# Performance work log

Measured on AMD Instinct MI355X. Metric: run time of the kernel, lower is better.

## Reference

```python
import jax, jax.numpy as jnp
import numpy as np

GRID_SIZE = 8
SPLINE_ORDER = 3  # cubic B-splines
GRID_MIN, GRID_MAX = -1.0, 1.0


def _make_grid():
    # Extended knot vector: grid_size + 2*order intervals -> G+2k+1 knots
    h = (GRID_MAX - GRID_MIN) / GRID_SIZE
    n = GRID_SIZE + 2 * SPLINE_ORDER + 1
    return jnp.asarray(GRID_MIN - SPLINE_ORDER * h + h * np.arange(n, dtype=np.float32))


def bspline_basis(x, grid, k):
    # x: (B, in) -> (B, in, G+k) via Cox-de Boor recursion
    x = x[..., None]
    b = ((x >= grid[:-1]) & (x < grid[1:])).astype(x.dtype)
    for p in range(1, k + 1):
        left = (x - grid[: -(p + 1)]) / (grid[p:-1] - grid[: -(p + 1)]) * b[..., :-1]
        right = (grid[p + 1:] - x) / (grid[p + 1:] - grid[1:-p]) * b[..., 1:]
        b = left + right
    return b


def setup_inputs() -> dict:
    key = jax.random.key(0)
    k1, k2, k3 = jax.random.split(key, 3)
    B, IN, OUT = 32768, 256, 256
    NB = GRID_SIZE + SPLINE_ORDER  # 11
    x = jax.random.normal(k1, (B, IN), dtype=jnp.float32)
    ln_gamma = jnp.ones((IN,), dtype=jnp.float32)
    ln_beta = jnp.zeros((IN,), dtype=jnp.float32)
    coeff = jax.random.normal(k2, (OUT, IN, NB), dtype=jnp.float32) * 0.1
    base_w = jax.random.normal(k3, (OUT, IN), dtype=jnp.float32) * (1.0 / np.sqrt(IN))
    return {"x": x, "ln_gamma": ln_gamma, "ln_beta": ln_beta, "coeff": coeff, "base_w": base_w}


def reference(x, ln_gamma, ln_beta, coeff, base_w):
    grid = _make_grid()
    # LayerNorm over in_features (eps = torch default 1e-5)
    mu = jnp.mean(x, axis=-1, keepdims=True)
    var = jnp.mean(jnp.square(x - mu), axis=-1, keepdims=True)
    normalized = (x - mu) * jax.lax.rsqrt(var + 1e-5) * ln_gamma + ln_beta
    # Spline branch: basis expansion (B, in, nb) contracted with coeff (out, in, nb)
    basis = bspline_basis(normalized, grid, SPLINE_ORDER)
    spline = jnp.einsum('bin,oin->bo', basis, coeff)
    # Base branch: SiLU(x) @ W^T (note: uses raw x, not normalized)
    base = jnp.einsum('bi,oi->bo', jax.nn.silu(x), base_w)
    return spline + base
```

## Files before the change

kernel.cpp:

```cpp
#include <hip/hip_runtime.h>
#include <hip/hip_bf16.h>

typedef _Float16 f16x8 __attribute__((ext_vector_type(8)));
typedef float f32x4 __attribute__((ext_vector_type(4)));

#define BM 128
#define BKH 96
#define NCHUNK 32
#define IN_F 256
#define OUT_F 256
#define KDIM 3072

__device__ inline void async_b16(const void* g, void* l) {
  __builtin_amdgcn_global_load_lds(
      (const __attribute__((address_space(1))) unsigned int*)g,
      (__attribute__((address_space(3))) unsigned int*)l, 16, 0, 0);
}

static __device__ inline unsigned pack2(float a, float b) {
  union { _Float16 h[2]; unsigned u; } t;
  t.h[0] = (_Float16)a;
  t.h[1] = (_Float16)b;
  return t.u;
}

__global__ __launch_bounds__(256) void prep_w(const float* __restrict__ coeff,
                                              const float* __restrict__ base_w,
                                              _Float16* __restrict__ W2F) {
  const int u   = blockIdx.x * 256 + threadIdx.x;
  const int c   = u / 3072;
  const int r   = u % 3072;
  const int bcb = r / 192;
  const int r2  = r % 192;
  const int g   = r2 / 64;
  const int ln  = r2 % 64;
  const int o   = bcb * 16 + (ln & 15);
  const int k8  = g * 4 + (ln >> 4);
  const int kh0 = c * 96 + k8 * 8;
  _Float16 h[8];
  #pragma unroll
  for (int e = 0; e < 8; ++e) {
    const int k = kh0 + e;
    const int i = k / 12, m = k % 12;
    const float v = (m == 11) ? base_w[o * IN_F + i] : coeff[(o * IN_F + i) * 11 + m];
    h[e] = (_Float16)v;
  }
  *(f16x8*)&W2F[(size_t)u * 8] = *(const f16x8*)h;
}

__global__ __launch_bounds__(512, 2) void kan_fused(const float* __restrict__ x,
                                                    const float* __restrict__ gamma,
                                                    const float* __restrict__ beta,
                                                    const _Float16* __restrict__ W2F,
                                                    float* __restrict__ out) {
  __shared__ _Float16 A0[24 * 512], A1[24 * 512];
  __shared__ _Float16 B0[48 * 512], B1[48 * 512];
  __shared__ float mu_s[BM], rs_s[BM];

  const int tid  = threadIdx.x;
  const int lane = tid & 63;
  const int wid  = tid >> 6;
  const int row0 = blockIdx.x * BM;

  for (int rr = wid; rr < BM; rr += 8) {
    const float4 v = *(const float4*)(x + (size_t)(row0 + rr) * IN_F + lane * 4);
    float s  = v.x + v.y + v.z + v.w;
    float sq = v.x * v.x + v.y * v.y + v.z * v.z + v.w * v.w;
    #pragma unroll
    for (int off = 32; off >= 1; off >>= 1) {
      s  += __shfl_xor(s, off);
      sq += __shfl_xor(sq, off);
    }
    if (lane == 0) {
      const float mu  = s * (1.0f / 256.0f);
      const float var = sq * (1.0f / 256.0f) - mu * mu;
      mu_s[rr] = mu;
      rs_s[rr] = 1.0f / sqrtf(var + 1e-5f);
    }
  }
  __syncthreads();

  const int wr   = wid >> 2;
  const int wc   = wid & 3;
  const int lrow = lane & 15;

  f32x4 acc[4][4] = {};

  const int plrow = tid & 15;
  const int pfq   = (tid >> 4) & 3;
  const int prb   = tid >> 6;
  const int prow  = prb * 16 + plrow;
  const float mu = mu_s[prow], rs = rs_s[prow];
  const float* xrow = x + (size_t)(row0 + prow) * IN_F + pfq * 2;
  const float* grow = gamma + pfq * 2;
  const float* brow = beta + pfq * 2;

  int aoff0, aoff1, aoff2;
  {
    const int k80 = pfq * 3 + 0, k81 = pfq * 3 + 1, k82 = pfq * 3 + 2;
    aoff0 = (prb * 3 + (k80 >> 2)) * 512 + (k80 & 3) * 128 + plrow * 8;
    aoff1 = (prb * 3 + (k81 >> 2)) * 512 + (k81 & 3) * 128 + plrow * 8;
    aoff2 = (prb * 3 + (k82 >> 2)) * 512 + (k82 & 3) * 128 + plrow * 8;
  }

  const char* const wsrc = (const char*)W2F + (size_t)wid * 6144 + (size_t)lane * 16;
  auto stageB = [&](int c, _Float16* Bb) {
    const char* gb = wsrc + (size_t)c * 49152;
    char* lb = (char*)Bb + wid * 6144;
    #pragma unroll
    for (int j = 0; j < 6; ++j)
      async_b16(gb + j * 1024, lb + j * 1024);
  };

  auto produce = [&](_Float16* buf, float2 xv, float2 gv, float2 bv) {
    unsigned R[12];
    #pragma unroll
    for (int q = 0; q < 2; ++q) {
      const float xr = q ? xv.y : xv.x;
      const float gq = q ? gv.y : gv.x;
      const float bq = q ? bv.y : bv.x;
      const float n  = (xr - mu) * rs * gq + bq;
      const float v  = (n + 1.75f) * 4.0f;
      const float fj = floorf(v);
      const float u  = v - fj;
      const float u2 = u * u, u3 = u2 * u;
      const float w0 = (1.0f / 6.0f) * (1.0f - 3.0f * u + 3.0f * u2 - u3);
      const float w1 = (1.0f / 6.0f) * (3.0f * u3 - 6.0f * u2 + 4.0f);
      const float w2 = (1.0f / 6.0f) * (-3.0f * u3 + 3.0f * u2 + 3.0f * u + 1.0f);
      const float w3 = (1.0f / 6.0f) * u3;
      const unsigned W0 = pack2(w0, w1);
      const unsigned W1 = pack2(w2, w3);
      const int p    = (int)fj - 3;
      const bool odd = (p & 1);
      const unsigned v0 = odd ? (W0 << 16) : W0;
      const unsigned v1 = odd ? ((W0 >> 16) | (W1 << 16)) : W1;
      const unsigned v2 = odd ? (W1 >> 16) : 0u;
      const int s0 = (v >= 0.0f && v < 14.0f) ? (p >> 1) : 99;
      const int s1 = s0 + 1, s2 = s0 + 2;
      #pragma unroll
      for (int k = 0; k < 6; ++k) {
        unsigned r = (k == s0) ? v0 : 0u;
        r = (k == s1) ? v1 : r;
        r = (k == s2) ? v2 : r;
        R[q * 6 + k] = r;
      }
      const float sl = xr * __builtin_amdgcn_rcpf(1.0f + __expf(-xr));
      R[q * 6 + 5] = (R[q * 6 + 5] & 0x0000FFFFu) | pack2(0.0f, sl);
    }
    *(f16x8*)&buf[aoff0] = *(const f16x8*)&R[0];
    *(f16x8*)&buf[aoff1] = *(const f16x8*)&R[4];
    *(f16x8*)&buf[aoff2] = *(const f16x8*)&R[8];
  };

  auto domfma = [&](const _Float16* Ab, const _Float16* Bb) {
    #pragma unroll
    for (int fk = 0; fk < 3; ++fk) {
      f16x8 a[4], b[4];
      #pragma unroll
      for (int fm = 0; fm < 4; ++fm)
        a[fm] = *(const f16x8*)&Ab[((wr * 4 + fm) * 3 + fk) * 512 + lane * 8];
      #pragma unroll
      for (int fn = 0; fn < 4; ++fn)
        b[fn] = *(const f16x8*)&Bb[((wc * 4 + fn) * 3 + fk) * 512 + lane * 8];
      #pragma unroll
      for (int fm = 0; fm < 4; ++fm)
        #pragma unroll
        for (int fn = 0; fn < 4; ++fn)
          acc[fm][fn] = __builtin_amdgcn_mfma_f32_16x16x32_f16(a[fm], b[fn], acc[fm][fn], 0, 0, 0);
    }
  };

  stageB(0, B0);
  float2 xv0 = *(const float2*)(xrow);
  float2 gv0 = *(const float2*)(grow);
  float2 bv0 = *(const float2*)(brow);
  float2 xv1 = *(const float2*)(xrow + 8);
  float2 gv1 = *(const float2*)(grow + 8);
  float2 bv1 = *(const float2*)(brow + 8);
  produce(A0, xv0, gv0, bv0);
  __syncthreads();

  for (int c = 0; c < NCHUNK; c += 2) {
    const int cp2 = (c + 2 < NCHUNK) ? (c + 2) : (NCHUNK - 1);
    const int cp3 = (c + 3 < NCHUNK) ? (c + 3) : (NCHUNK - 1);
    stageB(c + 1, B1);
    xv0 = *(const float2*)(xrow + cp2 * 8);
    gv0 = *(const float2*)(grow + cp2 * 8);
    bv0 = *(const float2*)(brow + cp2 * 8);
    if (wid & 1) { domfma(A0, B0); produce(A1, xv1, gv1, bv1); }
    else         { produce(A1, xv1, gv1, bv1); domfma(A0, B0); }
    __syncthreads();
    stageB(cp2, B0);
    xv1 = *(const float2*)(xrow + cp3 * 8);
    gv1 = *(const float2*)(grow + cp3 * 8);
    bv1 = *(const float2*)(brow + cp3 * 8);
    if (wid & 1) { domfma(A1, B1); produce(A0, xv0, gv0, bv0); }
    else         { produce(A0, xv0, gv0, bv0); domfma(A1, B1); }
    __syncthreads();
  }

  const int orow0 = row0 + wr * 64 + (lane >> 4) * 4;
  const int ocol0 = wc * 64 + lrow;
  #pragma unroll
  for (int fm = 0; fm < 4; ++fm)
    #pragma unroll
    for (int fn = 0; fn < 4; ++fn)
      #pragma unroll
      for (int r = 0; r < 4; ++r)
        out[(size_t)(orow0 + fm * 16 + r) * OUT_F + ocol0 + fn * 16] = acc[fm][fn][r];
}

extern "C" void kernel_launch(void* const* d_in, const int* in_sizes, int n_in,
                              void* d_out, int out_size, void* d_ws, size_t ws_size,
                              hipStream_t stream) {
  const float* x      = (const float*)d_in[0];
  const float* gamma  = (const float*)d_in[1];
  const float* beta   = (const float*)d_in[2];
  const float* coeff  = (const float*)d_in[3];
  const float* base_w = (const float*)d_in[4];
  float* out = (float*)d_out;
  _Float16* W2F = (_Float16*)d_ws;

  prep_w<<<dim3(384), dim3(256), 0, stream>>>(coeff, base_w, W2F);
  kan_fused<<<dim3(32768 / BM), dim3(512), 0, stream>>>(x, gamma, beta, W2F, out);
}
```

Baseline: 81.42 us.

## Load weight fragments directly from global into registers, bypassing LDS

Removes the LDS staging of the weight (B) tiles via global_load_lds. Each wave now loads its own B fragments straight from global memory into register double buffers (bA/bB), and the MFMA loop reads B from registers. This cuts LDS traffic and frees LDS, and the launch bound no longer requests 2 blocks per CU. In exchange, waves that share a column group load the same weights redundantly from global/L2, and register pressure rises by 24 f16x8 vectors, which may limit occupancy.

New measurement: 92.75 us. 1.14x slower.

```diff
diff --git a/kernel.cpp b/kernel.cpp
--- a/kernel.cpp
+++ b/kernel.cpp
@@ -5,17 +5,10 @@
 typedef float f32x4 __attribute__((ext_vector_type(4)));
 
 #define BM 128
-#define BKH 96
 #define NCHUNK 32
 #define IN_F 256
 #define OUT_F 256
 #define KDIM 3072
-
-__device__ inline void async_b16(const void* g, void* l) {
-  __builtin_amdgcn_global_load_lds(
-      (const __attribute__((address_space(1))) unsigned int*)g,
-      (__attribute__((address_space(3))) unsigned int*)l, 16, 0, 0);
-}
 
 static __device__ inline unsigned pack2(float a, float b) {
   union { _Float16 h[2]; unsigned u; } t;
@@ -48,13 +41,12 @@
   *(f16x8*)&W2F[(size_t)u * 8] = *(const f16x8*)h;
 }
 
-__global__ __launch_bounds__(512, 2) void kan_fused(const float* __restrict__ x,
-                                                    const float* __restrict__ gamma,
-                                                    const float* __restrict__ beta,
-                                                    const _Float16* __restrict__ W2F,
-                                                    float* __restrict__ out) {
+__global__ __launch_bounds__(512) void kan_fused(const float* __restrict__ x,
+                                                 const float* __restrict__ gamma,
+                                                 const float* __restrict__ beta,
+                                                 const _Float16* __restrict__ W2F,
+                                                 float* __restrict__ out) {
   __shared__ _Float16 A0[24 * 512], A1[24 * 512];
-  __shared__ _Float16 B0[48 * 512], B1[48 * 512];
   __shared__ float mu_s[BM], rs_s[BM];
 
   const int tid  = threadIdx.x;
@@ -103,13 +95,14 @@
     aoff2 = (prb * 3 + (k82 >> 2)) * 512 + (k82 & 3) * 128 + plrow * 8;
   }
 
-  const char* const wsrc = (const char*)W2F + (size_t)wid * 6144 + (size_t)lane * 16;
-  auto stageB = [&](int c, _Float16* Bb) {
-    const char* gb = wsrc + (size_t)c * 49152;
-    char* lb = (char*)Bb + wid * 6144;
-    #pragma unroll
-    for (int j = 0; j < 6; ++j)
-      async_b16(gb + j * 1024, lb + j * 1024);
+  const char* const wbsrc = (const char*)W2F + (size_t)wc * 12288 + (size_t)lane * 16;
+  auto loadB = [&](int c, f16x8* bf) {
+    const char* gb = wbsrc + (size_t)c * 49152;
+    #pragma unroll
+    for (int fk = 0; fk < 3; ++fk)
+      #pragma unroll
+      for (int fn = 0; fn < 4; ++fn)
+        bf[fk * 4 + fn] = *(const f16x8*)(gb + (fn * 3 + fk) * 1024);
   };
 
   auto produce = [&](_Float16* buf, float2 xv, float2 gv, float2 bv) {
@@ -152,25 +145,23 @@
     *(f16x8*)&buf[aoff2] = *(const f16x8*)&R[8];
   };
 
-  auto domfma = [&](const _Float16* Ab, const _Float16* Bb) {
+  auto domfma = [&](const _Float16* Ab, const f16x8* bf) {
     #pragma unroll
     for (int fk = 0; fk < 3; ++fk) {
-      f16x8 a[4], b[4];
+      f16x8 a[4];
       #pragma unroll
       for (int fm = 0; fm < 4; ++fm)
         a[fm] = *(const f16x8*)&Ab[((wr * 4 + fm) * 3 + fk) * 512 + lane * 8];
-      #pragma unroll
-      for (int fn = 0; fn < 4; ++fn)
-        b[fn] = *(const f16x8*)&Bb[((wc * 4 + fn) * 3 + fk) * 512 + lane * 8];
       #pragma unroll
       for (int fm = 0; fm < 4; ++fm)
         #pragma unroll
         for (int fn = 0; fn < 4; ++fn)
-          acc[fm][fn] = __builtin_amdgcn_mfma_f32_16x16x32_f16(a[fm], b[fn], acc[fm][fn], 0, 0, 0);
+          acc[fm][fn] = __builtin_amdgcn_mfma_f32_16x16x32_f16(a[fm], bf[fk * 4 + fn], acc[fm][fn], 0, 0, 0);
     }
   };
 
-  stageB(0, B0);
+  f16x8 bA[12], bB[12];
+  loadB(0, bA);
   float2 xv0 = *(const float2*)(xrow);
   float2 gv0 = *(const float2*)(grow);
   float2 bv0 = *(const float2*)(brow);
@@ -183,19 +174,19 @@
   for (int c = 0; c < NCHUNK; c += 2) {
     const int cp2 = (c + 2 < NCHUNK) ? (c + 2) : (NCHUNK - 1);
     const int cp3 = (c + 3 < NCHUNK) ? (c + 3) : (NCHUNK - 1);
-    stageB(c + 1, B1);
+    loadB(c + 1, bB);
     xv0 = *(const float2*)(xrow + cp2 * 8);
     gv0 = *(const float2*)(grow + cp2 * 8);
     bv0 = *(const float2*)(brow + cp2 * 8);
-    if (wid & 1) { domfma(A0, B0); produce(A1, xv1, gv1, bv1); }
-    else         { produce(A1, xv1, gv1, bv1); domfma(A0, B0); }
+    if (wid & 1) { domfma(A0, bA); produce(A1, xv1, gv1, bv1); }
+    else         { produce(A1, xv1, gv1, bv1); domfma(A0, bA); }
     __syncthreads();
-    stageB(cp2, B0);
+    loadB(cp2, bA);
     xv1 = *(const float2*)(xrow + cp3 * 8);
     gv1 = *(const float2*)(grow + cp3 * 8);
     bv1 = *(const float2*)(brow + cp3 * 8);
-    if (wid & 1) { domfma(A1, B1); produce(A0, xv0, gv0, bv0); }
-    else         { produce(A0, xv0, gv0, bv0); domfma(A1, B1); }
+    if (wid & 1) { domfma(A1, bB); produce(A0, xv0, gv0, bv0); }
+    else         { produce(A0, xv0, gv0, bv0); domfma(A1, bB); }
     __syncthreads();
   }
 
```

## Single-buffer LDS tiles to fit four blocks per CU with register-held A staging

Applied to the files above, without the earlier changes.

Replaces the double-buffered A and B shared-memory tiles with single buffers, halving LDS use, and raises the launch bound from 2 to 4 blocks per CU. The spline basis is computed into registers while the MFMAs run, then written to LDS after a barrier, and the next B chunk is loaded only after that barrier. This aims to hide latency through more resident waves instead of intra-block double buffering. In exchange there are twice as many barriers per chunk, the asynchronous B load is no longer overlapped with compute inside a block, and the tighter register budget may cause spills.

Result: slower. 137.9 us (+69.3%).

```diff
diff --git a/kernel.cpp b/kernel.cpp
--- a/kernel.cpp
+++ b/kernel.cpp
@@ -5,7 +5,6 @@
 typedef float f32x4 __attribute__((ext_vector_type(4)));
 
 #define BM 128
-#define BKH 96
 #define NCHUNK 32
 #define IN_F 256
 #define OUT_F 256
@@ -48,13 +47,13 @@
   *(f16x8*)&W2F[(size_t)u * 8] = *(const f16x8*)h;
 }
 
-__global__ __launch_bounds__(512, 2) void kan_fused(const float* __restrict__ x,
+__global__ __launch_bounds__(512, 4) void kan_fused(const float* __restrict__ x,
                                                     const float* __restrict__ gamma,
                                                     const float* __restrict__ beta,
                                                     const _Float16* __restrict__ W2F,
                                                     float* __restrict__ out) {
-  __shared__ _Float16 A0[24 * 512], A1[24 * 512];
-  __shared__ _Float16 B0[48 * 512], B1[48 * 512];
+  __shared__ _Float16 Abuf[24 * 512];
+  __shared__ _Float16 Bbuf[48 * 512];
   __shared__ float mu_s[BM], rs_s[BM];
 
   const int tid  = threadIdx.x;
@@ -104,16 +103,15 @@
   }
 
   const char* const wsrc = (const char*)W2F + (size_t)wid * 6144 + (size_t)lane * 16;
-  auto stageB = [&](int c, _Float16* Bb) {
+  char* const bdst = (char*)Bbuf + wid * 6144;
+  auto stageB = [&](int c) {
     const char* gb = wsrc + (size_t)c * 49152;
-    char* lb = (char*)Bb + wid * 6144;
     #pragma unroll
     for (int j = 0; j < 6; ++j)
-      async_b16(gb + j * 1024, lb + j * 1024);
-  };
-
-  auto produce = [&](_Float16* buf, float2 xv, float2 gv, float2 bv) {
-    unsigned R[12];
+      async_b16(gb + j * 1024, bdst + j * 1024);
+  };
+
+  auto produce_compute = [&](unsigned (&R)[12], float2 xv, float2 gv, float2 bv) {
     #pragma unroll
     for (int q = 0; q < 2; ++q) {
       const float xr = q ? xv.y : xv.x;
@@ -147,21 +145,24 @@
       const float sl = xr * __builtin_amdgcn_rcpf(1.0f + __expf(-xr));
       R[q * 6 + 5] = (R[q * 6 + 5] & 0x0000FFFFu) | pack2(0.0f, sl);
     }
-    *(f16x8*)&buf[aoff0] = *(const f16x8*)&R[0];
-    *(f16x8*)&buf[aoff1] = *(const f16x8*)&R[4];
-    *(f16x8*)&buf[aoff2] = *(const f16x8*)&R[8];
-  };
-
-  auto domfma = [&](const _Float16* Ab, const _Float16* Bb) {
+  };
+
+  auto writeA = [&](const unsigned (&R)[12]) {
+    *(f16x8*)&Abuf[aoff0] = *(const f16x8*)&R[0];
+    *(f16x8*)&Abuf[aoff1] = *(const f16x8*)&R[4];
+    *(f16x8*)&Abuf[aoff2] = *(const f16x8*)&R[8];
+  };
+
+  auto domfma = [&]() {
     #pragma unroll
     for (int fk = 0; fk < 3; ++fk) {
       f16x8 a[4], b[4];
       #pragma unroll
       for (int fm = 0; fm < 4; ++fm)
-        a[fm] = *(const f16x8*)&Ab[((wr * 4 + fm) * 3 + fk) * 512 + lane * 8];
+        a[fm] = *(const f16x8*)&Abuf[((wr * 4 + fm) * 3 + fk) * 512 + lane * 8];
       #pragma unroll
       for (int fn = 0; fn < 4; ++fn)
-        b[fn] = *(const f16x8*)&Bb[((wc * 4 + fn) * 3 + fk) * 512 + lane * 8];
+        b[fn] = *(const f16x8*)&Bbuf[((wc * 4 + fn) * 3 + fk) * 512 + lane * 8];
       #pragma unroll
       for (int fm = 0; fm < 4; ++fm)
         #pragma unroll
@@ -170,33 +171,46 @@
     }
   };
 
-  stageB(0, B0);
+  stageB(0);
   float2 xv0 = *(const float2*)(xrow);
   float2 gv0 = *(const float2*)(grow);
   float2 bv0 = *(const float2*)(brow);
   float2 xv1 = *(const float2*)(xrow + 8);
   float2 gv1 = *(const float2*)(grow + 8);
   float2 bv1 = *(const float2*)(brow + 8);
-  produce(A0, xv0, gv0, bv0);
+  unsigned R[12];
+  produce_compute(R, xv0, gv0, bv0);
+  writeA(R);
+  xv0 = *(const float2*)(xrow + 16);
+  gv0 = *(const float2*)(grow + 16);
+  bv0 = *(const float2*)(brow + 16);
   __syncthreads();
 
   for (int c = 0; c < NCHUNK; c += 2) {
-    const int cp2 = (c + 2 < NCHUNK) ? (c + 2) : (NCHUNK - 1);
-    const int cp3 = (c + 3 < NCHUNK) ? (c + 3) : (NCHUNK - 1);
-    stageB(c + 1, B1);
-    xv0 = *(const float2*)(xrow + cp2 * 8);
-    gv0 = *(const float2*)(grow + cp2 * 8);
-    bv0 = *(const float2*)(brow + cp2 * 8);
-    if (wid & 1) { domfma(A0, B0); produce(A1, xv1, gv1, bv1); }
-    else         { produce(A1, xv1, gv1, bv1); domfma(A0, B0); }
+    produce_compute(R, xv1, gv1, bv1);
+    domfma();
     __syncthreads();
-    stageB(cp2, B0);
-    xv1 = *(const float2*)(xrow + cp3 * 8);
-    gv1 = *(const float2*)(grow + cp3 * 8);
-    bv1 = *(const float2*)(brow + cp3 * 8);
-    if (wid & 1) { domfma(A1, B1); produce(A0, xv0, gv0, bv0); }
-    else         { produce(A0, xv0, gv0, bv0); domfma(A1, B1); }
+    writeA(R);
+    stageB(c + 1);
+    if (c + 3 < NCHUNK) {
+      xv1 = *(const float2*)(xrow + (c + 3) * 8);
+      gv1 = *(const float2*)(grow + (c + 3) * 8);
+      bv1 = *(const float2*)(brow + (c + 3) * 8);
+    }
     __syncthreads();
+    if (c + 2 < NCHUNK) produce_compute(R, xv0, gv0, bv0);
+    domfma();
+    __syncthreads();
+    if (c + 2 < NCHUNK) {
+      writeA(R);
+      stageB(c + 2);
+      if (c + 4 < NCHUNK) {
+        xv0 = *(const float2*)(xrow + (c + 4) * 8);
+        gv0 = *(const float2*)(grow + (c + 4) * 8);
+        bv0 = *(const float2*)(brow + (c + 4) * 8);
+      }
+      __syncthreads();
+    }
   }
 
   const int orow0 = row0 + wr * 64 + (lane >> 4) * 4;
```

## Double block size and dedicate half the waves to basis production and staging

Applied to the files above, without the earlier changes.

The fused KAN kernel now launches 1024-thread blocks. Only the first 8 waves compute the B-spline/SiLU A tiles and issue the async weight loads, while all 16 waves run MFMA on a 2x4 fragment tile instead of 4x4. The goal is more waves per CU to hide latency and a split of producer and MMA work across waves. The cost is that the non-producer waves sit idle at barriers during production. The launch bound of (1024,4) also forces a very tight VGPR budget, which risks register spills.

Result: faster. 76.11 us (-6.5%).

```diff
diff --git a/kernel.cpp b/kernel.cpp
--- a/kernel.cpp
+++ b/kernel.cpp
@@ -5,7 +5,6 @@
 typedef float f32x4 __attribute__((ext_vector_type(4)));
 
 #define BM 128
-#define BKH 96
 #define NCHUNK 32
 #define IN_F 256
 #define OUT_F 256
@@ -48,11 +47,11 @@
   *(f16x8*)&W2F[(size_t)u * 8] = *(const f16x8*)h;
 }
 
-__global__ __launch_bounds__(512, 2) void kan_fused(const float* __restrict__ x,
-                                                    const float* __restrict__ gamma,
-                                                    const float* __restrict__ beta,
-                                                    const _Float16* __restrict__ W2F,
-                                                    float* __restrict__ out) {
+__global__ __launch_bounds__(1024, 4) void kan_fused(const float* __restrict__ x,
+                                                     const float* __restrict__ gamma,
+                                                     const float* __restrict__ beta,
+                                                     const _Float16* __restrict__ W2F,
+                                                     float* __restrict__ out) {
   __shared__ _Float16 A0[24 * 512], A1[24 * 512];
   __shared__ _Float16 B0[48 * 512], B1[48 * 512];
   __shared__ float mu_s[BM], rs_s[BM];
@@ -62,7 +61,7 @@
   const int wid  = tid >> 6;
   const int row0 = blockIdx.x * BM;
 
-  for (int rr = wid; rr < BM; rr += 8) {
+  for (int rr = wid; rr < BM; rr += 16) {
     const float4 v = *(const float4*)(x + (size_t)(row0 + rr) * IN_F + lane * 4);
     float s  = v.x + v.y + v.z + v.w;
     float sq = v.x * v.x + v.y * v.y + v.z * v.z + v.w * v.w;
@@ -80,15 +79,16 @@
   }
   __syncthreads();
 
-  const int wr   = wid >> 2;
+  const int wr2  = wid >> 2;
   const int wc   = wid & 3;
   const int lrow = lane & 15;
 
-  f32x4 acc[4][4] = {};
-
+  f32x4 acc[2][4] = {};
+
+  const bool isprod = (wid < 8);
   const int plrow = tid & 15;
   const int pfq   = (tid >> 4) & 3;
-  const int prb   = tid >> 6;
+  const int prb   = (tid >> 6) & 7;
   const int prow  = prb * 16 + plrow;
   const float mu = mu_s[prow], rs = rs_s[prow];
   const float* xrow = x + (size_t)(row0 + prow) * IN_F + pfq * 2;
@@ -103,10 +103,10 @@
     aoff2 = (prb * 3 + (k82 >> 2)) * 512 + (k82 & 3) * 128 + plrow * 8;
   }
 
-  const char* const wsrc = (const char*)W2F + (size_t)wid * 6144 + (size_t)lane * 16;
+  const char* const wsrc = (const char*)W2F + (size_t)(wid & 7) * 6144 + (size_t)lane * 16;
   auto stageB = [&](int c, _Float16* Bb) {
     const char* gb = wsrc + (size_t)c * 49152;
-    char* lb = (char*)Bb + wid * 6144;
+    char* lb = (char*)Bb + (wid & 7) * 6144;
     #pragma unroll
     for (int j = 0; j < 6; ++j)
       async_b16(gb + j * 1024, lb + j * 1024);
@@ -155,54 +155,61 @@
   auto domfma = [&](const _Float16* Ab, const _Float16* Bb) {
     #pragma unroll
     for (int fk = 0; fk < 3; ++fk) {
-      f16x8 a[4], b[4];
-      #pragma unroll
-      for (int fm = 0; fm < 4; ++fm)
-        a[fm] = *(const f16x8*)&Ab[((wr * 4 + fm) * 3 + fk) * 512 + lane * 8];
+      f16x8 a[2], b[4];
+      #pragma unroll
+      for (int fm = 0; fm < 2; ++fm)
+        a[fm] = *(const f16x8*)&Ab[((wr2 * 2 + fm) * 3 + fk) * 512 + lane * 8];
       #pragma unroll
       for (int fn = 0; fn < 4; ++fn)
         b[fn] = *(const f16x8*)&Bb[((wc * 4 + fn) * 3 + fk) * 512 + lane * 8];
       #pragma unroll
-      for (int fm = 0; fm < 4; ++fm)
+      for (int fm = 0; fm < 2; ++fm)
         #pragma unroll
         for (int fn = 0; fn < 4; ++fn)
           acc[fm][fn] = __builtin_amdgcn_mfma_f32_16x16x32_f16(a[fm], b[fn], acc[fm][fn], 0, 0, 0);
     }
   };
 
-  stageB(0, B0);
-  float2 xv0 = *(const float2*)(xrow);
-  float2 gv0 = *(const float2*)(grow);
-  float2 bv0 = *(const float2*)(brow);
-  float2 xv1 = *(const float2*)(xrow + 8);
-  float2 gv1 = *(const float2*)(grow + 8);
-  float2 bv1 = *(const float2*)(brow + 8);
-  produce(A0, xv0, gv0, bv0);
+  float2 xv0 = {}, gv0 = {}, bv0 = {}, xv1 = {}, gv1 = {}, bv1 = {};
+  if (isprod) {
+    stageB(0, B0);
+    xv0 = *(const float2*)(xrow);
+    gv0 = *(const float2*)(grow);
+    bv0 = *(const float2*)(brow);
+    xv1 = *(const float2*)(xrow + 8);
+    gv1 = *(const float2*)(grow + 8);
+    bv1 = *(const float2*)(brow + 8);
+    produce(A0, xv0, gv0, bv0);
+  }
   __syncthreads();
 
   for (int c = 0; c < NCHUNK; c += 2) {
     const int cp2 = (c + 2 < NCHUNK) ? (c + 2) : (NCHUNK - 1);
     const int cp3 = (c + 3 < NCHUNK) ? (c + 3) : (NCHUNK - 1);
-    stageB(c + 1, B1);
-    xv0 = *(const float2*)(xrow + cp2 * 8);
-    gv0 = *(const float2*)(grow + cp2 * 8);
-    bv0 = *(const float2*)(brow + cp2 * 8);
-    if (wid & 1) { domfma(A0, B0); produce(A1, xv1, gv1, bv1); }
-    else         { produce(A1, xv1, gv1, bv1); domfma(A0, B0); }
+    if (isprod) {
+      stageB(c + 1, B1);
+      xv0 = *(const float2*)(xrow + cp2 * 8);
+      gv0 = *(const float2*)(grow + cp2 * 8);
+      bv0 = *(const float2*)(brow + cp2 * 8);
+      produce(A1, xv1, gv1, bv1);
+    }
+    domfma(A0, B0);
     __syncthreads();
-    stageB(cp2, B0);
-    xv1 = *(const float2*)(xrow + cp3 * 8);
-    gv1 = *(const float2*)(grow + cp3 * 8);
-    bv1 = *(const float2*)(brow + cp3 * 8);
-    if (wid & 1) { domfma(A1, B1); produce(A0, xv0, gv0, bv0); }
-    else         { produce(A0, xv0, gv0, bv0); domfma(A1, B1); }
+    if (isprod) {
+      stageB(cp2, B0);
+      xv1 = *(const float2*)(xrow + cp3 * 8);
+      gv1 = *(const float2*)(grow + cp3 * 8);
+      bv1 = *(const float2*)(brow + cp3 * 8);
+      produce(A0, xv0, gv0, bv0);
+    }
+    domfma(A1, B1);
     __syncthreads();
   }
 
-  const int orow0 = row0 + wr * 64 + (lane >> 4) * 4;
+  const int orow0 = row0 + wr2 * 32 + (lane >> 4) * 4;
   const int ocol0 = wc * 64 + lrow;
   #pragma unroll
-  for (int fm = 0; fm < 4; ++fm)
+  for (int fm = 0; fm < 2; ++fm)
     #pragma unroll
     for (int fn = 0; fn < 4; ++fn)
       #pragma unroll
@@ -222,5 +229,5 @@
   _Float16* W2F = (_Float16*)d_ws;
 
   prep_w<<<dim3(384), dim3(256), 0, stream>>>(coeff, base_w, W2F);
-  kan_fused<<<dim3(32768 / BM), dim3(512), 0, stream>>>(x, gamma, beta, W2F, out);
-}
+  kan_fused<<<dim3(32768 / BM), dim3(1024), 0, stream>>>(x, gamma, beta, W2F, out);
+}
```
